# Optimization experiments

Hardware: AMD Instinct MI355X
Metric: run time of the kernel (lower is better)

Reference implementation:

```python
import jax, jax.numpy as jnp
import numpy as np

EMBED_DIM = 512
NUM_HEADS = 8
HEAD_DIM = EMBED_DIM // NUM_HEADS
FFN_DIM = 4 * EMBED_DIM
B, S = 4, 2048
LN_EPS = 1e-5


def _linear_params(key, fan_in, fan_out):
    kw, kb = jax.random.split(key)
    bound = 1.0 / np.sqrt(fan_in)
    W = jax.random.uniform(kw, (fan_in, fan_out), jnp.float32, -bound, bound)
    b = jax.random.uniform(kb, (fan_out,), jnp.float32, -bound, bound)
    return W, b


def setup_inputs() -> dict:
    key = jax.random.key(0)
    ks = jax.random.split(key, 10)
    query = jax.random.normal(ks[0], (B, S, EMBED_DIM), jnp.float32)
    key_t = jax.random.normal(ks[1], (B, S, EMBED_DIM), jnp.float32)
    value = jax.random.normal(ks[2], (B, S, EMBED_DIM), jnp.float32)
    Wq, bq = _linear_params(ks[3], EMBED_DIM, EMBED_DIM)
    Wk, bk = _linear_params(ks[4], EMBED_DIM, EMBED_DIM)
    Wv, bv = _linear_params(ks[5], EMBED_DIM, EMBED_DIM)
    Wo, bo = _linear_params(ks[6], EMBED_DIM, EMBED_DIM)
    W1, b1 = _linear_params(ks[7], EMBED_DIM, FFN_DIM)
    W2, b2 = _linear_params(ks[8], FFN_DIM, EMBED_DIM)
    g1 = jnp.ones((EMBED_DIM,), jnp.float32); be1 = jnp.zeros((EMBED_DIM,), jnp.float32)
    g2 = jnp.ones((EMBED_DIM,), jnp.float32); be2 = jnp.zeros((EMBED_DIM,), jnp.float32)
    return dict(query=query, key=key_t, value=value,
                Wq=Wq, bq=bq, Wk=Wk, bk=bk, Wv=Wv, bv=bv, Wo=Wo, bo=bo,
                g1=g1, be1=be1, g2=g2, be2=be2,
                W1=W1, b1=b1, W2=W2, b2=b2)


def _layernorm(x, g, b):
    mu = jnp.mean(x, axis=-1, keepdims=True)
    var = jnp.mean(jnp.square(x - mu), axis=-1, keepdims=True)
    return (x - mu) * jax.lax.rsqrt(var + LN_EPS) * g + b


def reference(query, key, value, Wq, bq, Wk, bk, Wv, bv, Wo, bo,
              g1, be1, g2, be2, W1, b1, W2, b2):
    b_, s_ = query.shape[:2]
    # projections -> [B, H, S, Dh]
    Q = (query @ Wq + bq).reshape(b_, -1, NUM_HEADS, HEAD_DIM).transpose(0, 2, 1, 3)
    K = (key @ Wk + bk).reshape(b_, -1, NUM_HEADS, HEAD_DIM).transpose(0, 2, 1, 3)
    V = (value @ Wv + bv).reshape(b_, -1, NUM_HEADS, HEAD_DIM).transpose(0, 2, 1, 3)
    scores = jnp.einsum('bhqd,bhkd->bhqk', Q, K) / jnp.sqrt(jnp.float32(HEAD_DIM))
    attn = jax.nn.softmax(scores, axis=-1)  # dropout is eval-mode identity
    ctx = jnp.einsum('bhqk,bhkd->bhqd', attn, V)
    ctx = ctx.transpose(0, 2, 1, 3).reshape(b_, -1, EMBED_DIM)
    out = ctx @ Wo + bo
    out = _layernorm(query + out, g1, be1)
    ffn = jax.nn.gelu(out @ W1 + b1, approximate=False) @ W2 + b2
    return _layernorm(out + ffn, g2, be2)
```

## Files before the change

### kernel.cpp

```cpp
#include <hip/hip_runtime.h>
#include <hip/hip_bf16.h>
#include <math.h>

#define EMBED 512
#define NHEAD 8
#define HDIM 64
#define FFN 2048
#define BB 4
#define SS 2048
#define MROWS (BB*SS)
#define NB ((size_t)MROWS * EMBED)
#define LN_EPS 1e-5f

typedef __attribute__((ext_vector_type(8))) short short8;
typedef __attribute__((ext_vector_type(4))) float floatx4;

__device__ inline float bf2f(__hip_bfloat16 x) { return __bfloat162float(x); }
__device__ inline __hip_bfloat16 f2bf(float x) { return __float2bfloat16(x); }

__device__ inline float gelu_f(float x) {
    return 0.5f * x * (1.0f + erff(x * 0.70710678118654752f));
}

__device__ inline void async_copy16(const void* g, void* l) {
    __builtin_amdgcn_global_load_lds(
        (const __attribute__((address_space(1))) void*)g,
        (__attribute__((address_space(3))) void*)l, 16, 0, 0);
}

__global__ void detect_kernel(const void* __restrict__ q, int* __restrict__ flag) {
    const float* qf = (const float*)q;
    int lane = threadIdx.x;
    float v = qf[lane * 1024 + 7];
    bool ok = (v == v) && (fabsf(v) > 0x1p-40f) && (fabsf(v) < 0x1p40f);
    unsigned long long m = __ballot(ok);
    if (lane == 0) *flag = (__popcll(m) >= 32) ? 1 : 0;
}

__global__ __launch_bounds__(256) void cvt_qkv_kernel(
    const void* __restrict__ q, const void* __restrict__ k, const void* __restrict__ v,
    __hip_bfloat16* __restrict__ out, const int* __restrict__ dflag)
{
    const int f32 = *dflag;
    size_t pos = ((size_t)blockIdx.x * 256 + threadIdx.x) * 8;
    int sel = (int)(pos >> 22);
    size_t off = pos & (NB - 1);
    const void* src = sel == 0 ? q : sel == 1 ? k : v;
    if (f32) {
        const float* s = (const float*)src + off;
        float4 f0 = *reinterpret_cast<const float4*>(s);
        float4 f1 = *reinterpret_cast<const float4*>(s + 4);
        alignas(16) __hip_bfloat16 h[8] = {
            f2bf(f0.x), f2bf(f0.y), f2bf(f0.z), f2bf(f0.w),
            f2bf(f1.x), f2bf(f1.y), f2bf(f1.z), f2bf(f1.w)};
        *reinterpret_cast<uint4*>(out + pos) = *reinterpret_cast<const uint4*>(h);
    } else {
        *reinterpret_cast<uint4*>(out + pos) =
            *reinterpret_cast<const uint4*>((const __hip_bfloat16*)src + off);
    }
}

__global__ __launch_bounds__(256) void transpose_tile_kernel(
    const void* __restrict__ src, __hip_bfloat16* __restrict__ dst,
    int R, int C, const int* __restrict__ dflag)
{
    const int f32 = *dflag;
    const int r0 = blockIdx.x * 64, c0 = blockIdx.y * 64;
    __shared__ __hip_bfloat16 L[64][65];
    const int t = threadIdx.x;
    for (int c = t; c < 4096; c += 256) {
        int lr = c >> 6, lc = c & 63;
        __hip_bfloat16 v = f32 ? f2bf(((const float*)src)[(size_t)(r0 + lr) * C + c0 + lc])
                               : ((const __hip_bfloat16*)src)[(size_t)(r0 + lr) * C + c0 + lc];
        L[lr][lc] = v;
    }
    __syncthreads();
    for (int c = t; c < 4096; c += 256) {
        int lr = c >> 6, lc = c & 63;
        dst[(size_t)(c0 + lr) * R + r0 + lc] = L[lc][lr];
    }
}

__global__ __launch_bounds__(256) void transpose_tile4_kernel(
    const void* __restrict__ s0, const void* __restrict__ s1,
    const void* __restrict__ s2, const void* __restrict__ s3,
    __hip_bfloat16* __restrict__ dbase,
    const int* __restrict__ dflag)
{
    const int f32 = *dflag;
    const int which = blockIdx.z;
    const void* src = which == 0 ? s0 : which == 1 ? s1 : which == 2 ? s2 : s3;
    __hip_bfloat16* dst = dbase + (size_t)which * 512 * 512;
    const int r0 = blockIdx.x * 64, c0 = blockIdx.y * 64;
    __shared__ __hip_bfloat16 L[64][65];
    const int t = threadIdx.x;
    for (int c = t; c < 4096; c += 256) {
        int lr = c >> 6, lc = c & 63;
        __hip_bfloat16 v = f32 ? f2bf(((const float*)src)[(size_t)(r0 + lr) * 512 + c0 + lc])
                               : ((const __hip_bfloat16*)src)[(size_t)(r0 + lr) * 512 + c0 + lc];
        L[lr][lc] = v;
    }
    __syncthreads();
    for (int c = t; c < 4096; c += 256) {
        int lr = c >> 6, lc = c & 63;
        dst[(size_t)(c0 + lr) * 512 + r0 + lc] = L[lc][lr];
    }
}

template<int ACT>
__global__ __launch_bounds__(256) void gemm_bt_lds_kernel(
    const __hip_bfloat16* __restrict__ A,
    const __hip_bfloat16* __restrict__ Bt,
    const void* __restrict__ bias,
    __hip_bfloat16* __restrict__ C,
    int M, int N, int K, const int* __restrict__ dflag)
{
    const int f32 = *dflag;
    const int bm = blockIdx.x * 128;
    const int bn = blockIdx.y * 128;
    const int t = threadIdx.x;
    const int wave = t >> 6, lane = t & 63;
    const int wm = (wave >> 1) * 64, wn = (wave & 1) * 64;
    const int quad = lane >> 4, r = lane & 15;

    __shared__ alignas(16) __hip_bfloat16 As[128 * 32];
    __shared__ alignas(16) __hip_bfloat16 Bs[128 * 32];

    floatx4 acc[4][4];
    #pragma unroll
    for (int i = 0; i < 4; ++i)
        #pragma unroll
        for (int j = 0; j < 4; ++j)
            acc[i][j] = (floatx4){0.f, 0.f, 0.f, 0.f};

    const int c0 = wave * 128;

    for (int kt = 0; kt < K; kt += 32) {
        #pragma unroll
        for (int it = 0; it < 2; ++it) {
            int c = c0 + it * 64 + lane;
            int row = c >> 2, col = (c & 3) * 8;
            async_copy16(A + (size_t)(bm + row) * K + kt + col,
                         As + (size_t)(c0 + it * 64) * 8);
            async_copy16(Bt + (size_t)(bn + row) * K + kt + col,
                         Bs + (size_t)(c0 + it * 64) * 8);
        }
        __syncthreads();
        short8 af[4], bfr[4];
        #pragma unroll
        for (int i = 0; i < 4; ++i)
            af[i] = *reinterpret_cast<const short8*>(&As[(wm + i * 16 + r) * 32 + quad * 8]);
        #pragma unroll
        for (int j = 0; j < 4; ++j)
            bfr[j] = *reinterpret_cast<const short8*>(&Bs[(wn + j * 16 + r) * 32 + quad * 8]);
        #pragma unroll
        for (int i = 0; i < 4; ++i)
            #pragma unroll
            for (int j = 0; j < 4; ++j)
                acc[i][j] = __builtin_amdgcn_mfma_f32_16x16x32_bf16(af[i], bfr[j], acc[i][j], 0, 0, 0);
        __syncthreads();
    }

    #pragma unroll
    for (int j = 0; j < 4; ++j) {
        const int n = bn + wn + j * 16 + r;
        const float bvv = f32 ? ((const float*)bias)[n]
                              : bf2f(((const __hip_bfloat16*)bias)[n]);
        #pragma unroll
        for (int i = 0; i < 4; ++i) {
            #pragma unroll
            for (int v = 0; v < 4; ++v) {
                int m = bm + wm + i * 16 + quad * 4 + v;
                float x = acc[i][j][v] + bvv;
                if (ACT == 1) x = gelu_f(x);
                C[(size_t)m * N + n] = f2bf(x);
            }
        }
    }
}

__global__ __launch_bounds__(256) void gemm_qkv_fused_kernel(
    const __hip_bfloat16* __restrict__ Acat,
    const __hip_bfloat16* __restrict__ Wcat,
    const void* __restrict__ bq, const void* __restrict__ bk, const void* __restrict__ bv,
    __hip_bfloat16* __restrict__ Ocat,
    const int* __restrict__ dflag)
{
    const int f32 = *dflag;
    const int sel = blockIdx.x >> 6;
    const __hip_bfloat16* A = Acat + (size_t)sel * NB;
    const __hip_bfloat16* Bt = Wcat + (size_t)sel * 512 * 512;
    const void* bias = sel == 0 ? bq : sel == 1 ? bk : bv;
    __hip_bfloat16* C = Ocat + (size_t)sel * NB;

    const int bm = (blockIdx.x & 63) * 128;
    const int bn = blockIdx.y * 128;
    const int t = threadIdx.x;
    const int wave = t >> 6, lane = t & 63;
    const int wm = (wave >> 1) * 64, wn = (wave & 1) * 64;
    const int quad = lane >> 4, r = lane & 15;
    const int K = EMBED, N = EMBED;

    __shared__ alignas(16) __hip_bfloat16 As[128 * 32];
    __shared__ alignas(16) __hip_bfloat16 Bs[128 * 32];

    floatx4 acc[4][4];
    #pragma unroll
    for (int i = 0; i < 4; ++i)
        #pragma unroll
        for (int j = 0; j < 4; ++j)
            acc[i][j] = (floatx4){0.f, 0.f, 0.f, 0.f};

    const int c0 = wave * 128;

    for (int kt = 0; kt < K; kt += 32) {
        #pragma unroll
        for (int it = 0; it < 2; ++it) {
            int c = c0 + it * 64 + lane;
            int row = c >> 2, col = (c & 3) * 8;
            async_copy16(A + (size_t)(bm + row) * K + kt + col,
                         As + (size_t)(c0 + it * 64) * 8);
            async_copy16(Bt + (size_t)(bn + row) * K + kt + col,
                         Bs + (size_t)(c0 + it * 64) * 8);
        }
        __syncthreads();
        short8 af[4], bfr[4];
        #pragma unroll
        for (int i = 0; i < 4; ++i)
            af[i] = *reinterpret_cast<const short8*>(&As[(wm + i * 16 + r) * 32 + quad * 8]);
        #pragma unroll
        for (int j = 0; j < 4; ++j)
            bfr[j] = *reinterpret_cast<const short8*>(&Bs[(wn + j * 16 + r) * 32 + quad * 8]);
        #pragma unroll
        for (int i = 0; i < 4; ++i)
            #pragma unroll
            for (int j = 0; j < 4; ++j)
                acc[i][j] = __builtin_amdgcn_mfma_f32_16x16x32_bf16(af[i], bfr[j], acc[i][j], 0, 0, 0);
        __syncthreads();
    }

    #pragma unroll
    for (int j = 0; j < 4; ++j) {
        const int n = bn + wn + j * 16 + r;
        const float bvv = f32 ? ((const float*)bias)[n]
                              : bf2f(((const __hip_bfloat16*)bias)[n]);
        #pragma unroll
        for (int i = 0; i < 4; ++i) {
            #pragma unroll
            for (int v = 0; v < 4; ++v) {
                int m = bm + wm + i * 16 + quad * 4 + v;
                C[(size_t)m * N + n] = f2bf(acc[i][j][v] + bvv);
            }
        }
    }
}

__global__ __launch_bounds__(256) void vtrans_kernel(
    const __hip_bfloat16* __restrict__ Vb, __hip_bfloat16* __restrict__ Vt)
{
    const int bh = blockIdx.y;
    const int b = bh >> 3, h = bh & 7;
    const int s0 = blockIdx.x * 64;
    __shared__ alignas(16) __hip_bfloat16 L[64][72];
    const int t = threadIdx.x;
    for (int c = t; c < 512; c += 256) {
        int row = c >> 3, g = c & 7;
        *reinterpret_cast<uint4*>(&L[row][g * 8]) =
            *reinterpret_cast<const uint4*>(Vb + (size_t)(b * SS + s0 + row) * EMBED + h * 64 + g * 8);
    }
    __syncthreads();
    for (int c = t; c < 512; c += 256) {
        int d = c >> 3, g = c & 7;
        alignas(16) __hip_bfloat16 tmp[8];
        #pragma unroll
        for (int j = 0; j < 8; ++j) tmp[j] = L[g * 8 + j][d];
        *reinterpret_cast<uint4*>(Vt + ((size_t)bh * 64 + d) * SS + s0 + g * 8) =
            *reinterpret_cast<const uint4*>(tmp);
    }
}

__global__ __launch_bounds__(256) void attn_mfma_kernel(
    const __hip_bfloat16* __restrict__ Qg,
    const __hip_bfloat16* __restrict__ Kg,
    const __hip_bfloat16* __restrict__ Vt,
    __hip_bfloat16* __restrict__ ctx)
{
    const int bh = blockIdx.y;
    const int b = bh >> 3, h = bh & 7;
    const int q0 = blockIdx.x * 64;
    const int t = threadIdx.x;
    const int w = t >> 6, lane = t & 63;
    const int quad = lane >> 4, r = lane & 15;

    __shared__ alignas(16) __hip_bfloat16 Ks[2][64 * 32];
    __shared__ alignas(16) __hip_bfloat16 Vs[2][64 * 32];
    __shared__ alignas(16) __hip_bfloat16 Ps[4][16][72];

    const size_t bbase = (size_t)b * SS * EMBED;
    const size_t hoff = (size_t)h * HDIM;
    const size_t vtbase = (size_t)bh * HDIM * SS;

    short8 aq[2];
    {
        const __hip_bfloat16* qrow = Qg + bbase + (size_t)(q0 + w * 16 + r) * EMBED + hoff;
        short8 t0 = *reinterpret_cast<const short8*>(qrow + quad * 8);
        short8 t1 = *reinterpret_cast<const short8*>(qrow + 32 + quad * 8);
        #pragma unroll
        for (int i = 0; i < 8; ++i) {
            ((__hip_bfloat16*)&aq[0])[i] = f2bf(bf2f(((const __hip_bfloat16*)&t0)[i]) * 0.125f);
            ((__hip_bfloat16*)&aq[1])[i] = f2bf(bf2f(((const __hip_bfloat16*)&t1)[i]) * 0.125f);
        }
    }

    const int tensor = w >> 1;
    const int slab = w & 1;
    const int srow = lane >> 2;
    const int scol = (lane & 3) * 8;

    float m_run = -1e30f;
    float l_run = 0.f;
    floatx4 o_acc[4];
    #pragma unroll
    for (int nt = 0; nt < 4; ++nt) o_acc[nt] = (floatx4){0.f, 0.f, 0.f, 0.f};

    for (int kt = 0; kt < SS; kt += 64) {
        __syncthreads();
        if (tensor == 0) {
            #pragma unroll
            for (int g = 0; g < 4; ++g) {
                int row = g * 16 + srow;
                async_copy16(Kg + bbase + (size_t)(kt + row) * EMBED + hoff + slab * 32 + scol,
                             &Ks[slab][g * 512]);
            }
        } else {
            #pragma unroll
            for (int g = 0; g < 4; ++g) {
                int row = g * 16 + srow;
                async_copy16(Vt + vtbase + (size_t)row * SS + kt + slab * 32 + scol,
                             &Vs[slab][g * 512]);
            }
        }
        __syncthreads();

        floatx4 sc[4];
        #pragma unroll
        for (int nt = 0; nt < 4; ++nt) sc[nt] = (floatx4){0.f, 0.f, 0.f, 0.f};
        #pragma unroll
        for (int nt = 0; nt < 4; ++nt) {
            short8 ak0 = *reinterpret_cast<const short8*>(&Ks[0][(nt * 16 + r) * 32 + quad * 8]);
            short8 ak1 = *reinterpret_cast<const short8*>(&Ks[1][(nt * 16 + r) * 32 + quad * 8]);
            sc[nt] = __builtin_amdgcn_mfma_f32_16x16x32_bf16(ak0, aq[0], sc[nt], 0, 0, 0);
            sc[nt] = __builtin_amdgcn_mfma_f32_16x16x32_bf16(ak1, aq[1], sc[nt], 0, 0, 0);
        }

        float mt = fmaxf(fmaxf(fmaxf(sc[0][0], sc[0][1]), fmaxf(sc[0][2], sc[0][3])),
                         fmaxf(fmaxf(sc[1][0], sc[1][1]), fmaxf(sc[1][2], sc[1][3])));
        mt = fmaxf(mt, fmaxf(fmaxf(fmaxf(sc[2][0], sc[2][1]), fmaxf(sc[2][2], sc[2][3])),
                             fmaxf(fmaxf(sc[3][0], sc[3][1]), fmaxf(sc[3][2], sc[3][3]))));
        mt = fmaxf(mt, __shfl_xor(mt, 16, 64));
        mt = fmaxf(mt, __shfl_xor(mt, 32, 64));

        float mn = fmaxf(m_run, mt);
        float alpha = __expf(m_run - mn);
        m_run = mn;

        float ps = 0.f;
        #pragma unroll
        for (int nt = 0; nt < 4; ++nt) {
            float p0 = __expf(sc[nt][0] - mn), p1 = __expf(sc[nt][1] - mn);
            float p2 = __expf(sc[nt][2] - mn), p3 = __expf(sc[nt][3] - mn);
            ps += (p0 + p1) + (p2 + p3);
            alignas(8) __hip_bfloat16 pk[4] = {f2bf(p0), f2bf(p1), f2bf(p2), f2bf(p3)};
            *reinterpret_cast<uint2*>(&Ps[w][r][nt * 16 + quad * 4]) =
                *reinterpret_cast<const uint2*>(pk);
        }
        ps += __shfl_xor(ps, 16, 64);
        ps += __shfl_xor(ps, 32, 64);
        l_run = l_run * alpha + ps;

        #pragma unroll
        for (int v = 0; v < 4; ++v) {
            float av = __shfl(alpha, quad * 4 + v, 64);
            o_acc[0][v] *= av; o_acc[1][v] *= av;
            o_acc[2][v] *= av; o_acc[3][v] *= av;
        }

        short8 ap0 = *reinterpret_cast<const short8*>(&Ps[w][r][quad * 8]);
        short8 ap1 = *reinterpret_cast<const short8*>(&Ps[w][r][32 + quad * 8]);
        #pragma unroll
        for (int nt = 0; nt < 4; ++nt) {
            short8 bv0 = *reinterpret_cast<const short8*>(&Vs[0][(nt * 16 + r) * 32 + quad * 8]);
            short8 bv1 = *reinterpret_cast<const short8*>(&Vs[1][(nt * 16 + r) * 32 + quad * 8]);
            o_acc[nt] = __builtin_amdgcn_mfma_f32_16x16x32_bf16(ap0, bv0, o_acc[nt], 0, 0, 0);
            o_acc[nt] = __builtin_amdgcn_mfma_f32_16x16x32_bf16(ap1, bv1, o_acc[nt], 0, 0, 0);
        }
    }

    #pragma unroll
    for (int v = 0; v < 4; ++v) {
        float lv = __shfl(l_run, quad * 4 + v, 64);
        float inv = 1.0f / lv;
        int q = q0 + w * 16 + quad * 4 + v;
        __hip_bfloat16* orow = ctx + bbase + (size_t)q * EMBED + hoff;
        #pragma unroll
        for (int nt = 0; nt < 4; ++nt)
            orow[nt * 16 + r] = f2bf(o_acc[nt][v] * inv);
    }
}

__device__ inline float block_reduce_sum(float v, float* sbuf) {
    #pragma unroll
    for (int off = 32; off; off >>= 1) v += __shfl_xor(v, off, 64);
    int wave = threadIdx.x >> 6;
    if ((threadIdx.x & 63) == 0) sbuf[wave] = v;
    __syncthreads();
    float r = sbuf[0] + sbuf[1] + sbuf[2] + sbuf[3];
    __syncthreads();
    return r;
}

__global__ __launch_bounds__(256) void add_ln_kernel(
    const void* __restrict__ X,
    const __hip_bfloat16* __restrict__ Y,
    const void* __restrict__ g,
    const void* __restrict__ bt,
    void* __restrict__ out,
    int x_ext, int out_ext, const int* __restrict__ dflag)
{
    __shared__ float sbuf[4];
    const int f32 = *dflag;
    const bool x32 = (x_ext != 0) && (f32 != 0);
    const bool o32 = (out_ext != 0) && (f32 != 0);
    const int row = blockIdx.x;
    const size_t base = (size_t)row * EMBED;
    const int t = threadIdx.x;

    float xa = x32 ? ((const float*)X)[base + t]
                   : bf2f(((const __hip_bfloat16*)X)[base + t]);
    float xb = x32 ? ((const float*)X)[base + t + 256]
                   : bf2f(((const __hip_bfloat16*)X)[base + t + 256]);
    float x0 = xa + bf2f(Y[base + t]);
    float x1 = xb + bf2f(Y[base + t + 256]);
    float s = block_reduce_sum(x0 + x1, sbuf);
    float mu = s * (1.0f / EMBED);
    float d0 = x0 - mu, d1 = x1 - mu;
    float vs = block_reduce_sum(d0 * d0 + d1 * d1, sbuf);
    float rstd = rsqrtf(vs * (1.0f / EMBED) + LN_EPS);

    float g0 = f32 ? ((const float*)g)[t]        : bf2f(((const __hip_bfloat16*)g)[t]);
    float g1v = f32 ? ((const float*)g)[t + 256] : bf2f(((const __hip_bfloat16*)g)[t + 256]);
    float b0 = f32 ? ((const float*)bt)[t]        : bf2f(((const __hip_bfloat16*)bt)[t]);
    float b1v = f32 ? ((const float*)bt)[t + 256] : bf2f(((const __hip_bfloat16*)bt)[t + 256]);

    float o0 = d0 * rstd * g0 + b0;
    float o1 = d1 * rstd * g1v + b1v;
    if (o32) {
        ((float*)out)[base + t] = o0;
        ((float*)out)[base + t + 256] = o1;
    } else {
        ((__hip_bfloat16*)out)[base + t] = f2bf(o0);
        ((__hip_bfloat16*)out)[base + t + 256] = f2bf(o1);
    }
}

extern "C" void kernel_launch(void* const* d_in, const int* in_sizes, int n_in,
                              void* d_out, int out_size, void* d_ws, size_t ws_size,
                              hipStream_t stream)
{
    (void)in_sizes; (void)n_in; (void)out_size; (void)ws_size;

    const void* query = d_in[0];
    const void* keyi  = d_in[1];
    const void* vali  = d_in[2];
    const void* Wq = d_in[3];  const void* bq = d_in[4];
    const void* Wk = d_in[5];  const void* bk = d_in[6];
    const void* Wv = d_in[7];  const void* bv = d_in[8];
    const void* Wo = d_in[9];  const void* bo = d_in[10];
    const void* g1 = d_in[11]; const void* be1 = d_in[12];
    const void* g2 = d_in[13]; const void* be2 = d_in[14];
    const void* W1 = d_in[15]; const void* b1 = d_in[16];
    const void* W2 = d_in[17]; const void* b2 = d_in[18];

    int* dflag = (int*)d_ws;
    __hip_bfloat16* p = (__hip_bfloat16*)((char*)d_ws + 64);
    __hip_bfloat16* WqT = p;
    __hip_bfloat16* WoT = WqT + 3 * 512 * 512;
    __hip_bfloat16* W1T = WoT + 512 * 512;
    __hip_bfloat16* W2T = W1T + 512 * 2048;
    __hip_bfloat16* buf = W2T + 512 * 2048;
    __hip_bfloat16* qkvbf = buf;
    __hip_bfloat16* QKVo  = buf + 3 * NB;
    __hip_bfloat16* Qb = QKVo;
    __hip_bfloat16* Kb = QKVo + NB;
    __hip_bfloat16* Vb = QKVo + 2 * NB;
    __hip_bfloat16* Vt   = buf;
    __hip_bfloat16* ctx  = buf + NB;
    __hip_bfloat16* prj  = buf + 2 * NB;
    __hip_bfloat16* x1   = Qb;
    __hip_bfloat16* hbf  = Kb;
    __hip_bfloat16* prj2 = ctx;

    detect_kernel<<<1, 64, 0, stream>>>(query, dflag);

    cvt_qkv_kernel<<<(3 * NB / 8) / 256, 256, 0, stream>>>(query, keyi, vali, qkvbf, dflag);

    transpose_tile4_kernel<<<dim3(8, 8, 4), 256, 0, stream>>>(Wq, Wk, Wv, Wo, WqT, dflag);
    transpose_tile_kernel<<<dim3(8, 32), 256, 0, stream>>>(W1, W1T, 512, 2048, dflag);
    transpose_tile_kernel<<<dim3(32, 8), 256, 0, stream>>>(W2, W2T, 2048, 512, dflag);

    gemm_qkv_fused_kernel<<<dim3(192, 4), 256, 0, stream>>>(qkvbf, WqT, bq, bk, bv, QKVo, dflag);

    vtrans_kernel<<<dim3(SS / 64, BB * NHEAD), 256, 0, stream>>>(Vb, Vt);

    attn_mfma_kernel<<<dim3(SS / 64, BB * NHEAD), 256, 0, stream>>>(Qb, Kb, Vt, ctx);

    gemm_bt_lds_kernel<0><<<dim3(MROWS / 128, EMBED / 128), 256, 0, stream>>>(ctx, WoT, bo, prj, MROWS, EMBED, EMBED, dflag);
    add_ln_kernel<<<MROWS, 256, 0, stream>>>(query, prj, g1, be1, x1, 1, 0, dflag);

    gemm_bt_lds_kernel<1><<<dim3(MROWS / 128, FFN / 128), 256, 0, stream>>>(x1, W1T, b1, hbf, MROWS, FFN, EMBED, dflag);
    gemm_bt_lds_kernel<0><<<dim3(MROWS / 128, EMBED / 128), 256, 0, stream>>>(hbf, W2T, b2, prj2, MROWS, EMBED, FFN, dflag);
    add_ln_kernel<<<MROWS, 256, 0, stream>>>(x1, prj2, g2, be2, d_out, 0, 1, dflag);
}
```

Baseline: 384.1 us.

## Split attention and FFN2 reduction over two K halves to raise occupancy

Attention runs as a split-KV (flash-decoding style) pass over two halves of the sequence, writing unnormalized partial outputs plus per-row max and sum, and a new combine kernel merges them. The FFN down-projection GEMM is split-K over two halves with partial outputs summed (plus bias) inside a new fused add+LayerNorm kernel. The first residual LayerNorm now reads the bf16-converted query instead of the original input. This doubles grid size for the low-block-count kernels (256 GEMM tiles, 1024 attention blocks) to fill more CUs, at the cost of extra partial-buffer traffic, an extra launch, and bf16 rounding of unnormalized partials.

```diff
diff --git a/kernel.cpp b/kernel.cpp
--- a/kernel.cpp
+++ b/kernel.cpp
@@ -107,17 +107,23 @@
     }
 }
 
-template<int ACT>
+template<int ACT, int BIAS>
 __global__ __launch_bounds__(256) void gemm_bt_lds_kernel(
     const __hip_bfloat16* __restrict__ A,
     const __hip_bfloat16* __restrict__ Bt,
     const void* __restrict__ bias,
     __hip_bfloat16* __restrict__ C,
-    int M, int N, int K, const int* __restrict__ dflag)
+    int M, int N, int K, int ksplit, const int* __restrict__ dflag)
 {
     const int f32 = *dflag;
     const int bm = blockIdx.x * 128;
     const int bn = blockIdx.y * 128;
+    int kbeg = 0, kend = K;
+    if (BIAS == 0) {
+        kbeg = blockIdx.z * ksplit;
+        kend = kbeg + ksplit;
+        C += (size_t)blockIdx.z * NB;
+    }
     const int t = threadIdx.x;
     const int wave = t >> 6, lane = t & 63;
     const int wm = (wave >> 1) * 64, wn = (wave & 1) * 64;
@@ -135,7 +141,7 @@
 
     const int c0 = wave * 128;
 
-    for (int kt = 0; kt < K; kt += 32) {
+    for (int kt = kbeg; kt < kend; kt += 32) {
         #pragma unroll
         for (int it = 0; it < 2; ++it) {
             int c = c0 + it * 64 + lane;
@@ -164,8 +170,9 @@
     #pragma unroll
     for (int j = 0; j < 4; ++j) {
         const int n = bn + wn + j * 16 + r;
-        const float bvv = f32 ? ((const float*)bias)[n]
-                              : bf2f(((const __hip_bfloat16*)bias)[n]);
+        float bvv = 0.f;
+        if (BIAS) bvv = f32 ? ((const float*)bias)[n]
+                            : bf2f(((const __hip_bfloat16*)bias)[n]);
         #pragma unroll
         for (int i = 0; i < 4; ++i) {
             #pragma unroll
@@ -283,11 +290,14 @@
     const __hip_bfloat16* __restrict__ Qg,
     const __hip_bfloat16* __restrict__ Kg,
     const __hip_bfloat16* __restrict__ Vt,
-    __hip_bfloat16* __restrict__ ctx)
+    __hip_bfloat16* __restrict__ Apart0,
+    __hip_bfloat16* __restrict__ Apart1,
+    float2* __restrict__ ml)
 {
     const int bh = blockIdx.y;
     const int b = bh >> 3, h = bh & 7;
     const int q0 = blockIdx.x * 64;
+    const int z = blockIdx.z;
     const int t = threadIdx.x;
     const int w = t >> 6, lane = t & 63;
     const int quad = lane >> 4, r = lane & 15;
@@ -323,7 +333,8 @@
     #pragma unroll
     for (int nt = 0; nt < 4; ++nt) o_acc[nt] = (floatx4){0.f, 0.f, 0.f, 0.f};
 
-    for (int kt = 0; kt < SS; kt += 64) {
+    const int kbeg = z * (SS / 2), kend = kbeg + SS / 2;
+    for (int kt = kbeg; kt < kend; kt += 64) {
         __syncthreads();
         if (tensor == 0) {
             #pragma unroll
@@ -396,15 +407,57 @@
         }
     }
 
+    __hip_bfloat16* Ap = z == 0 ? Apart0 : Apart1;
     #pragma unroll
     for (int v = 0; v < 4; ++v) {
-        float lv = __shfl(l_run, quad * 4 + v, 64);
-        float inv = 1.0f / lv;
         int q = q0 + w * 16 + quad * 4 + v;
-        __hip_bfloat16* orow = ctx + bbase + (size_t)q * EMBED + hoff;
+        __hip_bfloat16* orow = Ap + bbase + (size_t)q * EMBED + hoff;
         #pragma unroll
         for (int nt = 0; nt < 4; ++nt)
-            orow[nt * 16 + r] = f2bf(o_acc[nt][v] * inv);
+            orow[nt * 16 + r] = f2bf(o_acc[nt][v]);
+    }
+    if (lane < 16) {
+        ml[((size_t)z * 32 + bh) * SS + q0 + w * 16 + r] = make_float2(m_run, l_run);
+    }
+}
+
+__global__ __launch_bounds__(256) void attn_combine_kernel(
+    const __hip_bfloat16* __restrict__ Apart0,
+    const __hip_bfloat16* __restrict__ Apart1,
+    const float2* __restrict__ ml,
+    __hip_bfloat16* __restrict__ ctx)
+{
+    const int bh = blockIdx.y;
+    const int b = bh >> 3, h = bh & 7;
+    const int q0 = blockIdx.x * 64;
+    const int t = threadIdx.x;
+    __shared__ float w0[64], w1[64], winv[64];
+
+    if (t < 64) {
+        float2 ml0 = ml[(size_t)bh * SS + q0 + t];
+        float2 ml1 = ml[((size_t)32 + bh) * SS + q0 + t];
+        float m = fmaxf(ml0.x, ml1.x);
+        float a0 = __expf(ml0.x - m), a1 = __expf(ml1.x - m);
+        float denom = a0 * ml0.y + a1 * ml1.y;
+        w0[t] = a0; w1[t] = a1; winv[t] = 1.0f / denom;
+    }
+    __syncthreads();
+
+    const size_t base = (size_t)b * SS * EMBED + (size_t)h * HDIM;
+    for (int c = t; c < 512; c += 256) {
+        int q = c >> 3, d8 = (c & 7) * 8;
+        size_t off = base + (size_t)(q0 + q) * EMBED + d8;
+        short8 a0v = *reinterpret_cast<const short8*>(Apart0 + off);
+        short8 a1v = *reinterpret_cast<const short8*>(Apart1 + off);
+        float s0 = w0[q], s1 = w1[q], si = winv[q];
+        alignas(16) __hip_bfloat16 o[8];
+        #pragma unroll
+        for (int j = 0; j < 8; ++j) {
+            float x0 = bf2f(((const __hip_bfloat16*)&a0v)[j]);
+            float x1 = bf2f(((const __hip_bfloat16*)&a1v)[j]);
+            o[j] = f2bf((s0 * x0 + s1 * x1) * si);
+        }
+        *reinterpret_cast<uint4*>(ctx + off) = *reinterpret_cast<const uint4*>(o);
     }
 }
 
@@ -420,27 +473,21 @@
 }
 
 __global__ __launch_bounds__(256) void add_ln_kernel(
-    const void* __restrict__ X,
+    const __hip_bfloat16* __restrict__ X,
     const __hip_bfloat16* __restrict__ Y,
     const void* __restrict__ g,
     const void* __restrict__ bt,
-    void* __restrict__ out,
-    int x_ext, int out_ext, const int* __restrict__ dflag)
+    __hip_bfloat16* __restrict__ out,
+    const int* __restrict__ dflag)
 {
     __shared__ float sbuf[4];
     const int f32 = *dflag;
-    const bool x32 = (x_ext != 0) && (f32 != 0);
-    const bool o32 = (out_ext != 0) && (f32 != 0);
     const int row = blockIdx.x;
     const size_t base = (size_t)row * EMBED;
     const int t = threadIdx.x;
 
-    float xa = x32 ? ((const float*)X)[base + t]
-                   : bf2f(((const __hip_bfloat16*)X)[base + t]);
-    float xb = x32 ? ((const float*)X)[base + t + 256]
-                   : bf2f(((const __hip_bfloat16*)X)[base + t + 256]);
-    float x0 = xa + bf2f(Y[base + t]);
-    float x1 = xb + bf2f(Y[base + t + 256]);
+    float x0 = bf2f(X[base + t]) + bf2f(Y[base + t]);
+    float x1 = bf2f(X[base + t + 256]) + bf2f(Y[base + t + 256]);
     float s = block_reduce_sum(x0 + x1, sbuf);
     float mu = s * (1.0f / EMBED);
     float d0 = x0 - mu, d1 = x1 - mu;
@@ -452,9 +499,44 @@
     float b0 = f32 ? ((const float*)bt)[t]        : bf2f(((const __hip_bfloat16*)bt)[t]);
     float b1v = f32 ? ((const float*)bt)[t + 256] : bf2f(((const __hip_bfloat16*)bt)[t + 256]);
 
+    out[base + t]       = f2bf(d0 * rstd * g0 + b0);
+    out[base + t + 256] = f2bf(d1 * rstd * g1v + b1v);
+}
+
+__global__ __launch_bounds__(256) void add_ln_split_kernel(
+    const __hip_bfloat16* __restrict__ X,
+    const __hip_bfloat16* __restrict__ Y0,
+    const __hip_bfloat16* __restrict__ Y1,
+    const void* __restrict__ bias,
+    const void* __restrict__ g,
+    const void* __restrict__ bt,
+    void* __restrict__ out,
+    const int* __restrict__ dflag)
+{
+    __shared__ float sbuf[4];
+    const int f32 = *dflag;
+    const int row = blockIdx.x;
+    const size_t base = (size_t)row * EMBED;
+    const int t = threadIdx.x;
+
+    float bb0 = f32 ? ((const float*)bias)[t]       : bf2f(((const __hip_bfloat16*)bias)[t]);
+    float bb1 = f32 ? ((const float*)bias)[t + 256] : bf2f(((const __hip_bfloat16*)bias)[t + 256]);
+    float x0 = bf2f(X[base + t]) + bf2f(Y0[base + t]) + bf2f(Y1[base + t]) + bb0;
+    float x1 = bf2f(X[base + t + 256]) + bf2f(Y0[base + t + 256]) + bf2f(Y1[base + t + 256]) + bb1;
+    float s = block_reduce_sum(x0 + x1, sbuf);
+    float mu = s * (1.0f / EMBED);
+    float d0 = x0 - mu, d1 = x1 - mu;
+    float vs = block_reduce_sum(d0 * d0 + d1 * d1, sbuf);
+    float rstd = rsqrtf(vs * (1.0f / EMBED) + LN_EPS);
+
+    float g0 = f32 ? ((const float*)g)[t]        : bf2f(((const __hip_bfloat16*)g)[t]);
+    float g1v = f32 ? ((const float*)g)[t + 256] : bf2f(((const __hip_bfloat16*)g)[t + 256]);
+    float b0 = f32 ? ((const float*)bt)[t]        : bf2f(((const __hip_bfloat16*)bt)[t]);
+    float b1v = f32 ? ((const float*)bt)[t + 256] : bf2f(((const __hip_bfloat16*)bt)[t + 256]);
+
     float o0 = d0 * rstd * g0 + b0;
     float o1 = d1 * rstd * g1v + b1v;
-    if (o32) {
+    if (f32) {
         ((float*)out)[base + t] = o0;
         ((float*)out)[base + t + 256] = o1;
     } else {
@@ -488,17 +570,20 @@
     __hip_bfloat16* W1T = WoT + 512 * 512;
     __hip_bfloat16* W2T = W1T + 512 * 2048;
     __hip_bfloat16* buf = W2T + 512 * 2048;
-    __hip_bfloat16* qkvbf = buf;
-    __hip_bfloat16* QKVo  = buf + 3 * NB;
+    __hip_bfloat16* qkvbf  = buf;
+    __hip_bfloat16* QKVo   = buf + 3 * NB;
     __hip_bfloat16* Qb = QKVo;
     __hip_bfloat16* Kb = QKVo + NB;
     __hip_bfloat16* Vb = QKVo + 2 * NB;
-    __hip_bfloat16* Vt   = buf;
-    __hip_bfloat16* ctx  = buf + NB;
-    __hip_bfloat16* prj  = buf + 2 * NB;
-    __hip_bfloat16* x1   = Qb;
-    __hip_bfloat16* hbf  = Kb;
-    __hip_bfloat16* prj2 = ctx;
+    __hip_bfloat16* Vt     = buf + 1 * NB;
+    __hip_bfloat16* Apart0 = buf + 2 * NB;
+    __hip_bfloat16* Apart1 = buf + 6 * NB;
+    float2*         mlbuf  = (float2*)(buf + 7 * NB);
+    __hip_bfloat16* ctx    = buf + 3 * NB;
+    __hip_bfloat16* prj    = buf + 4 * NB;
+    __hip_bfloat16* x1     = buf + 5 * NB;
+    __hip_bfloat16* hbf    = buf + 1 * NB;
+    __hip_bfloat16* Ypart  = buf + 6 * NB;
 
     detect_kernel<<<1, 64, 0, stream>>>(query, dflag);
 
@@ -512,12 +597,19 @@
 
     vtrans_kernel<<<dim3(SS / 64, BB * NHEAD), 256, 0, stream>>>(Vb, Vt);
 
-    attn_mfma_kernel<<<dim3(SS / 64, BB * NHEAD), 256, 0, stream>>>(Qb, Kb, Vt, ctx);
-
-    gemm_bt_lds_kernel<0><<<dim3(MROWS / 128, EMBED / 128), 256, 0, stream>>>(ctx, WoT, bo, prj, MROWS, EMBED, EMBED, dflag);
-    add_ln_kernel<<<MROWS, 256, 0, stream>>>(query, prj, g1, be1, x1, 1, 0, dflag);
-
-    gemm_bt_lds_kernel<1><<<dim3(MROWS / 128, FFN / 128), 256, 0, stream>>>(x1, W1T, b1, hbf, MROWS, FFN, EMBED, dflag);
-    gemm_bt_lds_kernel<0><<<dim3(MROWS / 128, EMBED / 128), 256, 0, stream>>>(hbf, W2T, b2, prj2, MROWS, EMBED, FFN, dflag);
-    add_ln_kernel<<<MROWS, 256, 0, stream>>>(x1, prj2, g2, be2, d_out, 0, 1, dflag);
-}
+    attn_mfma_kernel<<<dim3(SS / 64, BB * NHEAD, 2), 256, 0, stream>>>(
+        Qb, Kb, Vt, Apart0, Apart1, mlbuf);
+    attn_combine_kernel<<<dim3(SS / 64, BB * NHEAD), 256, 0, stream>>>(
+        Apart0, Apart1, mlbuf, ctx);
+
+    gemm_bt_lds_kernel<0, 1><<<dim3(MROWS / 128, EMBED / 128), 256, 0, stream>>>(
+        ctx, WoT, bo, prj, MROWS, EMBED, EMBED, 0, dflag);
+    add_ln_kernel<<<MROWS, 256, 0, stream>>>(qkvbf, prj, g1, be1, x1, dflag);
+
+    gemm_bt_lds_kernel<1, 1><<<dim3(MROWS / 128, FFN / 128), 256, 0, stream>>>(
+        x1, W1T, b1, hbf, MROWS, FFN, EMBED, 0, dflag);
+    gemm_bt_lds_kernel<0, 0><<<dim3(MROWS / 128, EMBED / 128, 2), 256, 0, stream>>>(
+        hbf, W2T, nullptr, Ypart, MROWS, EMBED, FFN, FFN / 2, dflag);
+    add_ln_split_kernel<<<MROWS, 256, 0, stream>>>(
+        x1, Ypart, Ypart + NB, b2, g2, be2, d_out, dflag);
+}
```

New measurement: 387.6 us. About the same (+0.9%).
